# Kernel tuning notes

Hardware: AMD Instinct MI355X
Metric: run time of the kernel (lower is better)

The kernel has to match this reference:

```python
import jax, jax.numpy as jnp
import numpy as np

HEAD_SIZE = 64
INPUT_SIZE = 1024
B, T = 4, 4096


def setup_inputs() -> dict:
    key = jax.random.key(0)
    ks = jax.random.split(key, 7)
    s = 1.0 / np.sqrt(INPUT_SIZE)
    return {
        "x": jax.random.normal(ks[0], (B, T, INPUT_SIZE), dtype=jnp.float32),
        "Wk": jax.random.uniform(ks[1], (INPUT_SIZE, HEAD_SIZE), jnp.float32, -s, s),
        "bk": jax.random.uniform(ks[2], (HEAD_SIZE,), jnp.float32, -s, s),
        "Wq": jax.random.uniform(ks[3], (INPUT_SIZE, HEAD_SIZE), jnp.float32, -s, s),
        "bq": jax.random.uniform(ks[4], (HEAD_SIZE,), jnp.float32, -s, s),
        "Wv": jax.random.uniform(ks[5], (INPUT_SIZE, HEAD_SIZE), jnp.float32, -s, s),
        "bv": jax.random.uniform(ks[6], (HEAD_SIZE,), jnp.float32, -s, s),
    }


def reference(x, Wk, bk, Wq, bq, Wv, bv) -> jnp.ndarray:
    # x: [B, T, D]
    Tlen = x.shape[1]
    k = x @ Wk + bk          # [B, T, H]
    q = x @ Wq + bq          # [B, T, H]
    v = x @ Wv + bv          # [B, T, H]
    scale = 1.0 / jnp.sqrt(jnp.float32(HEAD_SIZE))
    # NOTE: original computes k @ q^T (not q @ k^T) -- keep that exact math.
    w = jnp.einsum("bth,bsh->bts", k, q) * scale  # [B, T, T]
    causal = jnp.tril(jnp.ones((Tlen, Tlen), dtype=bool))
    w = jnp.where(causal, w, -jnp.inf)
    w = jax.nn.softmax(w, axis=-1)
    out = jnp.einsum("bts,bsh->bth", w, v)        # [B, T, H]
    return out
```

## Files before the change

### kernel.cpp

```cpp
#include <hip/hip_runtime.h>
#include <hip/hip_bf16.h>
#include <stdint.h>

typedef __attribute__((ext_vector_type(8))) short short8;
typedef __attribute__((ext_vector_type(4))) float floatx4;

#define HD 64
#define D_IN 1024
#define TLEN 4096
#define NB 4
#define PPB 144
#define LDP 72
#define SL2E 0.18033688011112042f
#define WSZ 196608

__device__ __forceinline__ short f2bf(float f) {
    union { float f; uint32_t u; } v{f};
    uint32_t u = v.u;
    uint32_t r = (u + 0x7FFFu + ((u >> 16) & 1u)) >> 16;
    return (short)r;
}

__device__ __forceinline__ float bf2f(short s) {
    union { uint32_t u; float f; } v;
    v.u = ((uint32_t)(uint16_t)s) << 16;
    return v.f;
}

__device__ __forceinline__ uint32_t pk2(float a, float b) {
    __hip_bfloat162 h = __float22bfloat162_rn(float2{a, b});
    union { __hip_bfloat162 h; uint32_t u; } c{h};
    return c.u;
}

__device__ __forceinline__ void ld_lds16(const void* g, void* l) {
    __builtin_amdgcn_global_load_lds(
        (const __attribute__((address_space(1))) uint32_t*)g,
        (__attribute__((address_space(3))) uint32_t*)l, 16, 0, 0);
}

__global__ __launch_bounds__(256) void prep_w(const float* __restrict__ Wk,
                                              const float* __restrict__ Wq,
                                              const float* __restrict__ Wv,
                                              short* __restrict__ wt) {
    int i = blockIdx.x * 256 + threadIdx.x;
    int j  = i & 7;
    int l  = (i >> 3) & 63;
    int ks = (i >> 9) & 1;
    int rest = i >> 10;
    int f  = rest % 12;
    int kt = rest / 12;
    int mat = f >> 2, nt = f & 3;
    int n = nt * 16 + (l & 15);
    int k = kt * 64 + ks * 32 + (l >> 4) * 8 + j;
    const float* W = (mat == 0) ? Wk : ((mat == 1) ? Wq : Wv);
    wt[i] = f2bf(W[(size_t)k * 64 + n]);
}

__global__ __launch_bounds__(256) void proj(const float* __restrict__ x,
                                            const float* __restrict__ bk,
                                            const float* __restrict__ bq,
                                            const float* __restrict__ bv,
                                            const short* __restrict__ wt,
                                            short* __restrict__ ko,
                                            short* __restrict__ qo,
                                            short* __restrict__ vt) {
    __shared__ float xs[4][2048];

    int tid = threadIdx.x;
    int wave = tid >> 6, lane = tid & 63;
    int quad = lane >> 4, l16 = lane & 15;
    int row0 = blockIdx.x * 32;
    int wbase = tid & ~63;

    floatx4 acc[2][3];
#pragma unroll
    for (int mt = 0; mt < 2; mt++)
#pragma unroll
        for (int fi = 0; fi < 3; fi++) acc[mt][fi] = (floatx4){0.f, 0.f, 0.f, 0.f};

    auto stage = [&](int kt, int buf) {
#pragma unroll
        for (int it = 0; it < 2; it++) {
            int s = it * 256 + tid;
            int r = s >> 4, p = s & 15;
            int c = (((p >> 1) ^ (r & 7)) << 1) | (p & 1);
            ld_lds16(x + (size_t)(row0 + r) * D_IN + kt * 64 + c * 4,
                     &xs[buf][(it * 256 + wbase) * 4]);
        }
    };

    const short* wv0 = wt + (size_t)(((wave * 3) * 2) * 64 + lane) * 8;

    auto wload = [&](int kt, short8 (&wf)[3][2]) {
#pragma unroll
        for (int fi = 0; fi < 3; fi++)
#pragma unroll
            for (int ks = 0; ks < 2; ks++)
                wf[fi][ks] = *reinterpret_cast<const short8*>(
                    wv0 + (size_t)kt * 12288 + (size_t)((fi * 2 + ks) * 64) * 8);
    };

    auto body = [&](int kt, short8 (&wcur)[3][2]) {
        int buf = kt & 3;
#pragma unroll
        for (int ks = 0; ks < 2; ks++) {
            short8 av[2];
#pragma unroll
            for (int mt = 0; mt < 2; mt++) {
                int r = mt * 16 + l16;
                int g = ks * 4 + quad;
                const float4* pp = reinterpret_cast<const float4*>(
                    &xs[buf][r * 64 + ((g ^ (r & 7)) << 1) * 4]);
                float4 f0 = pp[0], f1 = pp[1];
                union { uint32_t u[4]; short8 s; } cv;
                cv.u[0] = pk2(f0.x, f0.y); cv.u[1] = pk2(f0.z, f0.w);
                cv.u[2] = pk2(f1.x, f1.y); cv.u[3] = pk2(f1.z, f1.w);
                av[mt] = cv.s;
            }
#pragma unroll
            for (int fi = 0; fi < 3; fi++)
#pragma unroll
                for (int mt = 0; mt < 2; mt++)
                    acc[mt][fi] = __builtin_amdgcn_mfma_f32_16x16x32_bf16(av[mt], wcur[fi][ks], acc[mt][fi], 0, 0, 0);
        }
    };

    short8 wA[3][2], wB[3][2];
    wload(0, wA);
    stage(0, 0); stage(1, 1); stage(2, 2);

    auto step = [&](int kt, short8 (&wcur)[3][2], short8 (&wnxt)[3][2]) {
        wload(kt + 1, wnxt);
        asm volatile("s_waitcnt vmcnt(8)" ::: "memory");
        __builtin_amdgcn_s_barrier();
        if (kt + 3 < 16) stage(kt + 3, (kt + 3) & 3);
        body(kt, wcur);
    };

    for (int kt2 = 0; kt2 < 14; kt2 += 2) {
        step(kt2, wA, wB);
        step(kt2 + 1, wB, wA);
    }
    wload(15, wB);
    asm volatile("s_waitcnt vmcnt(6)" ::: "memory");
    __builtin_amdgcn_s_barrier();
    body(14, wA);
    asm volatile("s_waitcnt vmcnt(0)" ::: "memory");
    __builtin_amdgcn_s_barrier();
    body(15, wB);

#pragma unroll
    for (int fi = 0; fi < 3; fi++) {
        int f = wave * 3 + fi;
        int mat = f >> 2, nt = f & 3;
        int col = nt * 16 + l16;
        const float* bias = (mat == 0) ? bk : ((mat == 1) ? bq : bv);
        float bb = bias[col];
#pragma unroll
        for (int mt = 0; mt < 2; mt++)
#pragma unroll
            for (int reg = 0; reg < 4; reg++) {
                float v = acc[mt][fi][reg] + bb;
                int row = row0 + mt * 16 + quad * 4 + reg;
                if (mat == 0) ko[(size_t)row * HD + col] = f2bf(v * SL2E);
                else if (mat == 1) qo[(size_t)row * HD + col] = f2bf(v);
                else {
                    int bt = row >> 12, tl = row & 4095;
                    vt[(size_t)bt * HD * TLEN + (size_t)col * TLEN + tl] = f2bf(v);
                }
            }
    }
}

template<int SPLIT>
__global__ __launch_bounds__(256) void attn_kern(const short* __restrict__ kb,
                                                 const short* __restrict__ qb,
                                                 const short* __restrict__ vtw,
                                                 short* __restrict__ pO,
                                                 float* __restrict__ pL,
                                                 float* __restrict__ out) {
    __shared__ short Ks[2][4096];
    __shared__ short Vs[2][4096];
    __shared__ short Ps[128 * LDP];

    int tid = threadIdx.x;
    int wave = tid >> 6, lane = tid & 63;
    int quad = lane >> 4, l16 = lane & 15;
    int wbase = tid & ~63;
    int batch = blockIdx.y;

    int tile, j0, j1, slot = 0, nparts = 1;
    if (SPLIT) {
        int bx = blockIdx.x;
        int t = 0, accb = 0;
        for (;;) { int p = (2 * t + 9) >> 3; if (bx < accb + p) break; accb += p; ++t; }
        tile = t;
        j0 = (bx - accb) * 8;
        int je = j0 + 8, lim = 2 * tile + 2;
        j1 = je < lim ? je : lim;
        slot = batch * PPB + bx;
        nparts = (2 * tile + 9) >> 3;
    } else {
        tile = 31 - blockIdx.x;
        j0 = 0; j1 = 2 * tile + 2;
    }
    int t0 = tile * 128;
    int jd = 2 * tile;
    size_t base = (size_t)batch * TLEN * HD;
    const short* vbase = vtw + (size_t)batch * HD * TLEN;

    short8 kf[2][2];
#pragma unroll
    for (int mt = 0; mt < 2; mt++) {
        int trow = t0 + wave * 32 + mt * 16 + l16;
#pragma unroll
        for (int ks = 0; ks < 2; ks++)
            kf[mt][ks] = *reinterpret_cast<const short8*>(kb + base + (size_t)trow * HD + ks * 32 + quad * 8);
    }

    floatx4 o_acc[2][4];
#pragma unroll
    for (int mt = 0; mt < 2; mt++)
#pragma unroll
        for (int ht = 0; ht < 4; ht++) o_acc[mt][ht] = (floatx4){0.f, 0.f, 0.f, 0.f};
    float l_p[2] = {0.f, 0.f};

    auto stage = [&](int j, int buf) {
        int s0 = j * 64;
#pragma unroll
        for (int it = 0; it < 2; it++) {
            int s = it * 256 + tid;
            int r = s >> 3, c = (s & 7) ^ (r & 7);
            ld_lds16(qb + base + (size_t)(s0 + r) * HD + c * 8,
                     &Ks[buf][(it * 256 + wbase) * 8]);
            ld_lds16(vbase + (size_t)r * TLEN + s0 + c * 8,
                     &Vs[buf][(it * 256 + wbase) * 8]);
        }
    };

    stage(j0, 0);
    for (int j = j0; j < j1; ++j) {
        int buf = (j - j0) & 1;
        __syncthreads();
        if (j + 1 < j1) stage(j + 1, buf ^ 1);

        if (j == jd + 1 && wave < 2) continue;

        floatx4 sacc[2][4];
#pragma unroll
        for (int mt = 0; mt < 2; mt++)
#pragma unroll
            for (int nt = 0; nt < 4; nt++) sacc[mt][nt] = (floatx4){0.f, 0.f, 0.f, 0.f};
#pragma unroll
        for (int ks = 0; ks < 2; ks++)
#pragma unroll
            for (int nt = 0; nt < 4; nt++) {
                int r = nt * 16 + l16, g = ks * 4 + quad;
                short8 a = *reinterpret_cast<const short8*>(
                    &Ks[buf][r * 64 + (g ^ (r & 7)) * 8]);
#pragma unroll
                for (int mt = 0; mt < 2; mt++)
                    sacc[mt][nt] = __builtin_amdgcn_mfma_f32_16x16x32_bf16(a, kf[mt][ks], sacc[mt][nt], 0, 0, 0);
            }

        float pv[2][4][4];
#pragma unroll
        for (int mt = 0; mt < 2; mt++)
#pragma unroll
            for (int nt = 0; nt < 4; nt++)
#pragma unroll
                for (int reg = 0; reg < 4; reg++)
                    pv[mt][nt][reg] = __builtin_amdgcn_exp2f(sacc[mt][nt][reg]);
        if (j >= jd) {
            int s0 = j * 64;
#pragma unroll
            for (int mt = 0; mt < 2; mt++) {
                int t_g = t0 + wave * 32 + mt * 16 + l16;
#pragma unroll
                for (int nt = 0; nt < 4; nt++) {
                    int s_g = s0 + nt * 16 + quad * 4;
#pragma unroll
                    for (int reg = 0; reg < 4; reg++)
                        if (s_g + reg > t_g) pv[mt][nt][reg] = 0.f;
                }
            }
        }
#pragma unroll
        for (int mt = 0; mt < 2; mt++) {
            l_p[mt] += ((pv[mt][0][0] + pv[mt][0][1]) + (pv[mt][0][2] + pv[mt][0][3]))
                     + ((pv[mt][1][0] + pv[mt][1][1]) + (pv[mt][1][2] + pv[mt][1][3]))
                     + ((pv[mt][2][0] + pv[mt][2][1]) + (pv[mt][2][2] + pv[mt][2][3]))
                     + ((pv[mt][3][0] + pv[mt][3][1]) + (pv[mt][3][2] + pv[mt][3][3]));
#pragma unroll
            for (int nt = 0; nt < 4; nt++) {
                union { uint32_t u[2]; uint64_t q; } w;
                w.u[0] = pk2(pv[mt][nt][0], pv[mt][nt][1]);
                w.u[1] = pk2(pv[mt][nt][2], pv[mt][nt][3]);
                int row = wave * 32 + mt * 16 + l16;
                *reinterpret_cast<uint64_t*>(&Ps[row * LDP + nt * 16 + quad * 4]) = w.q;
            }
        }

#pragma unroll
        for (int ks = 0; ks < 2; ks++) {
            short8 a[2];
#pragma unroll
            for (int mt = 0; mt < 2; mt++)
                a[mt] = *reinterpret_cast<const short8*>(
                    &Ps[(wave * 32 + mt * 16 + l16) * LDP + ks * 32 + quad * 8]);
#pragma unroll
            for (int ht = 0; ht < 4; ht++) {
                int r = ht * 16 + l16, g = ks * 4 + quad;
                short8 b = *reinterpret_cast<const short8*>(
                    &Vs[buf][r * 64 + (g ^ (r & 7)) * 8]);
#pragma unroll
                for (int mt = 0; mt < 2; mt++)
                    o_acc[mt][ht] = __builtin_amdgcn_mfma_f32_16x16x32_bf16(a[mt], b, o_acc[mt][ht], 0, 0, 0);
            }
        }
    }

#pragma unroll
    for (int mt = 0; mt < 2; mt++) {
        l_p[mt] += __shfl_xor(l_p[mt], 16);
        l_p[mt] += __shfl_xor(l_p[mt], 32);
    }

    if (SPLIT && nparts > 1) {
        short* po = pO + (size_t)slot * 8192;
#pragma unroll
        for (int mt = 0; mt < 2; mt++)
#pragma unroll
            for (int ht = 0; ht < 4; ht++)
#pragma unroll
                for (int reg = 0; reg < 4; reg++) {
                    int lr = wave * 32 + mt * 16 + quad * 4 + reg;
                    po[lr * 64 + ht * 16 + l16] = f2bf(o_acc[mt][ht][reg]);
                }
        if (quad == 0) {
#pragma unroll
            for (int mt = 0; mt < 2; mt++)
                pL[(size_t)slot * 128 + wave * 32 + mt * 16 + l16] = l_p[mt];
        }
    } else {
#pragma unroll
        for (int mt = 0; mt < 2; mt++) {
#pragma unroll
            for (int reg = 0; reg < 4; reg++) {
                float L = __shfl(l_p[mt], quad * 4 + reg, 64);
                float inv = 1.0f / L;
                int t = t0 + wave * 32 + mt * 16 + quad * 4 + reg;
#pragma unroll
                for (int ht = 0; ht < 4; ht++)
                    out[base + (size_t)t * HD + ht * 16 + l16] = o_acc[mt][ht][reg] * inv;
            }
        }
    }
}

__global__ __launch_bounds__(256) void attn_combine(const short* __restrict__ pO,
                                                    const float* __restrict__ pL,
                                                    float* __restrict__ out) {
    int tile = blockIdx.x + 4, batch = blockIdx.y, rq = blockIdx.z;
    int nparts = (2 * tile + 9) >> 3;
    int a = tile >> 2, r = tile & 3;
    int slot0 = batch * PPB + 2 * a * (a + 1) + r * (a + 1);
    int t = threadIdx.x;
    int off = rq * 2048 + t * 8;
    int row = off >> 6;
    int col0 = off & 63;

    float L = 0.f;
    float acc[8];
#pragma unroll
    for (int i = 0; i < 8; i++) acc[i] = 0.f;

    for (int p = 0; p < nparts; ++p) {
        int slot = slot0 + p;
        L += pL[(size_t)slot * 128 + row];
        short8 v = *reinterpret_cast<const short8*>(pO + (size_t)slot * 8192 + off);
#pragma unroll
        for (int i = 0; i < 8; i++) acc[i] += bf2f(v[i]);
    }
    float inv = 1.0f / L;
    float4* dstp = reinterpret_cast<float4*>(out + (size_t)batch * TLEN * HD +
                                             (size_t)(tile * 128 + row) * HD + col0);
#pragma unroll
    for (int c = 0; c < 2; c++) {
        float4 v;
        v.x = acc[c * 4 + 0] * inv; v.y = acc[c * 4 + 1] * inv;
        v.z = acc[c * 4 + 2] * inv; v.w = acc[c * 4 + 3] * inv;
        dstp[c] = v;
    }
}

extern "C" void kernel_launch(void* const* d_in, const int* in_sizes, int n_in,
                              void* d_out, int out_size, void* d_ws, size_t ws_size,
                              hipStream_t stream) {
    const float* x  = (const float*)d_in[0];
    const float* Wk = (const float*)d_in[1];
    const float* bk = (const float*)d_in[2];
    const float* Wq = (const float*)d_in[3];
    const float* bq = (const float*)d_in[4];
    const float* Wv = (const float*)d_in[5];
    const float* bv = (const float*)d_in[6];
    float* out = (float*)d_out;

    const size_t nrow = (size_t)NB * TLEN;
    short* ko = (short*)d_ws;
    short* qo = ko + nrow * HD;
    short* vt = qo + nrow * HD;
    short* wt = vt + nrow * HD;
    short* pO = wt + WSZ;
    float* pL = (float*)(pO + (size_t)NB * PPB * 8192);
    size_t need = (size_t)((char*)(pL + (size_t)NB * PPB * 128) - (char*)d_ws);

    prep_w<<<768, 256, 0, stream>>>(Wk, Wq, Wv, wt);
    proj<<<512, 256, 0, stream>>>(x, bk, bq, bv, wt, ko, qo, vt);
    if (ws_size >= need) {
        attn_kern<1><<<dim3(PPB, NB), 256, 0, stream>>>(ko, qo, vt, pO, pL, out);
        attn_combine<<<dim3(28, NB, 4), 256, 0, stream>>>(pO, pL, out);
    } else {
        attn_kern<0><<<dim3(32, NB), 256, 0, stream>>>(ko, qo, vt, nullptr, nullptr, out);
    }
}
```

Measured before the change: 149.8 us.

## Triple-buffer K/V tiles in attention with explicit vmcnt waits

Moves the attention kernel's K/V staging to dynamic shared memory with three slots and prefetches two tiles ahead instead of one. The __syncthreads is replaced by a targeted s_waitcnt vmcnt plus s_barrier so only the tile needed now must have landed. The aim is to hide more global load latency in the short per-block loops. In exchange it uses more LDS per block and depends on a hand-coded vmcnt count matching the number of loads issued per stage.

```diff
diff --git a/kernel.cpp b/kernel.cpp
--- a/kernel.cpp
+++ b/kernel.cpp
@@ -13,6 +13,7 @@
 #define LDP 72
 #define SL2E 0.18033688011112042f
 #define WSZ 196608
+#define ATTN_LDS (3 * 16384 + 128 * LDP * 2)
 
 __device__ __forceinline__ short f2bf(float f) {
     union { float f; uint32_t u; } v{f};
@@ -180,15 +181,14 @@
                                                  short* __restrict__ pO,
                                                  float* __restrict__ pL,
                                                  float* __restrict__ out) {
-    __shared__ short Ks[2][4096];
-    __shared__ short Vs[2][4096];
-    __shared__ short Ps[128 * LDP];
+    extern __shared__ char asmem[];
 
     int tid = threadIdx.x;
     int wave = tid >> 6, lane = tid & 63;
     int quad = lane >> 4, l16 = lane & 15;
     int wbase = tid & ~63;
     int batch = blockIdx.y;
+    short* Ps = (short*)(asmem + 3 * 16384);
 
     int tile, j0, j1, slot = 0, nparts = 1;
     if (SPLIT) {
@@ -226,99 +226,110 @@
         for (int ht = 0; ht < 4; ht++) o_acc[mt][ht] = (floatx4){0.f, 0.f, 0.f, 0.f};
     float l_p[2] = {0.f, 0.f};
 
-    auto stage = [&](int j, int buf) {
+    auto stage = [&](int j, int sl) {
+        short* Kd = (short*)(asmem + sl * 16384);
+        short* Vd = (short*)(asmem + sl * 16384 + 8192);
         int s0 = j * 64;
 #pragma unroll
         for (int it = 0; it < 2; it++) {
             int s = it * 256 + tid;
             int r = s >> 3, c = (s & 7) ^ (r & 7);
             ld_lds16(qb + base + (size_t)(s0 + r) * HD + c * 8,
-                     &Ks[buf][(it * 256 + wbase) * 8]);
+                     Kd + (it * 256 + wbase) * 8);
             ld_lds16(vbase + (size_t)r * TLEN + s0 + c * 8,
-                     &Vs[buf][(it * 256 + wbase) * 8]);
+                     Vd + (it * 256 + wbase) * 8);
         }
     };
 
     stage(j0, 0);
+    if (j0 + 1 < j1) stage(j0 + 1, 1);
+    int sl = 0, sn = 2;
     for (int j = j0; j < j1; ++j) {
-        int buf = (j - j0) & 1;
-        __syncthreads();
-        if (j + 1 < j1) stage(j + 1, buf ^ 1);
-
-        if (j == jd + 1 && wave < 2) continue;
-
-        floatx4 sacc[2][4];
-#pragma unroll
-        for (int mt = 0; mt < 2; mt++)
-#pragma unroll
-            for (int nt = 0; nt < 4; nt++) sacc[mt][nt] = (floatx4){0.f, 0.f, 0.f, 0.f};
-#pragma unroll
-        for (int ks = 0; ks < 2; ks++)
-#pragma unroll
-            for (int nt = 0; nt < 4; nt++) {
-                int r = nt * 16 + l16, g = ks * 4 + quad;
-                short8 a = *reinterpret_cast<const short8*>(
-                    &Ks[buf][r * 64 + (g ^ (r & 7)) * 8]);
+        if (j + 1 < j1) asm volatile("s_waitcnt vmcnt(4)" ::: "memory");
+        else            asm volatile("s_waitcnt vmcnt(0)" ::: "memory");
+        __builtin_amdgcn_s_barrier();
+        __builtin_amdgcn_sched_barrier(0);
+        if (j + 2 < j1) stage(j + 2, sn);
+
+        if (!(j == jd + 1 && wave < 2)) {
+            const short* Kc = (const short*)(asmem + sl * 16384);
+            const short* Vc = (const short*)(asmem + sl * 16384 + 8192);
+
+            floatx4 sacc[2][4];
+#pragma unroll
+            for (int mt = 0; mt < 2; mt++)
+#pragma unroll
+                for (int nt = 0; nt < 4; nt++) sacc[mt][nt] = (floatx4){0.f, 0.f, 0.f, 0.f};
+#pragma unroll
+            for (int ks = 0; ks < 2; ks++)
+#pragma unroll
+                for (int nt = 0; nt < 4; nt++) {
+                    int r = nt * 16 + l16, g = ks * 4 + quad;
+                    short8 a = *reinterpret_cast<const short8*>(
+                        Kc + r * 64 + (g ^ (r & 7)) * 8);
+#pragma unroll
+                    for (int mt = 0; mt < 2; mt++)
+                        sacc[mt][nt] = __builtin_amdgcn_mfma_f32_16x16x32_bf16(a, kf[mt][ks], sacc[mt][nt], 0, 0, 0);
+                }
+
+            float pv[2][4][4];
+#pragma unroll
+            for (int mt = 0; mt < 2; mt++)
+#pragma unroll
+                for (int nt = 0; nt < 4; nt++)
+#pragma unroll
+                    for (int reg = 0; reg < 4; reg++)
+                        pv[mt][nt][reg] = __builtin_amdgcn_exp2f(sacc[mt][nt][reg]);
+            if (j >= jd) {
+                int s0 = j * 64;
+#pragma unroll
+                for (int mt = 0; mt < 2; mt++) {
+                    int t_g = t0 + wave * 32 + mt * 16 + l16;
+#pragma unroll
+                    for (int nt = 0; nt < 4; nt++) {
+                        int s_g = s0 + nt * 16 + quad * 4;
+#pragma unroll
+                        for (int reg = 0; reg < 4; reg++)
+                            if (s_g + reg > t_g) pv[mt][nt][reg] = 0.f;
+                    }
+                }
+            }
+#pragma unroll
+            for (int mt = 0; mt < 2; mt++) {
+                l_p[mt] += ((pv[mt][0][0] + pv[mt][0][1]) + (pv[mt][0][2] + pv[mt][0][3]))
+                         + ((pv[mt][1][0] + pv[mt][1][1]) + (pv[mt][1][2] + pv[mt][1][3]))
+                         + ((pv[mt][2][0] + pv[mt][2][1]) + (pv[mt][2][2] + pv[mt][2][3]))
+                         + ((pv[mt][3][0] + pv[mt][3][1]) + (pv[mt][3][2] + pv[mt][3][3]));
+#pragma unroll
+                for (int nt = 0; nt < 4; nt++) {
+                    union { uint32_t u[2]; uint64_t q; } w;
+                    w.u[0] = pk2(pv[mt][nt][0], pv[mt][nt][1]);
+                    w.u[1] = pk2(pv[mt][nt][2], pv[mt][nt][3]);
+                    int row = wave * 32 + mt * 16 + l16;
+                    *reinterpret_cast<uint64_t*>(&Ps[row * LDP + nt * 16 + quad * 4]) = w.q;
+                }
+            }
+
+#pragma unroll
+            for (int ks = 0; ks < 2; ks++) {
+                short8 a[2];
 #pragma unroll
                 for (int mt = 0; mt < 2; mt++)
-                    sacc[mt][nt] = __builtin_amdgcn_mfma_f32_16x16x32_bf16(a, kf[mt][ks], sacc[mt][nt], 0, 0, 0);
-            }
-
-        float pv[2][4][4];
-#pragma unroll
-        for (int mt = 0; mt < 2; mt++)
-#pragma unroll
-            for (int nt = 0; nt < 4; nt++)
-#pragma unroll
-                for (int reg = 0; reg < 4; reg++)
-                    pv[mt][nt][reg] = __builtin_amdgcn_exp2f(sacc[mt][nt][reg]);
-        if (j >= jd) {
-            int s0 = j * 64;
-#pragma unroll
-            for (int mt = 0; mt < 2; mt++) {
-                int t_g = t0 + wave * 32 + mt * 16 + l16;
-#pragma unroll
-                for (int nt = 0; nt < 4; nt++) {
-                    int s_g = s0 + nt * 16 + quad * 4;
-#pragma unroll
-                    for (int reg = 0; reg < 4; reg++)
-                        if (s_g + reg > t_g) pv[mt][nt][reg] = 0.f;
-                }
-            }
-        }
-#pragma unroll
-        for (int mt = 0; mt < 2; mt++) {
-            l_p[mt] += ((pv[mt][0][0] + pv[mt][0][1]) + (pv[mt][0][2] + pv[mt][0][3]))
-                     + ((pv[mt][1][0] + pv[mt][1][1]) + (pv[mt][1][2] + pv[mt][1][3]))
-                     + ((pv[mt][2][0] + pv[mt][2][1]) + (pv[mt][2][2] + pv[mt][2][3]))
-                     + ((pv[mt][3][0] + pv[mt][3][1]) + (pv[mt][3][2] + pv[mt][3][3]));
-#pragma unroll
-            for (int nt = 0; nt < 4; nt++) {
-                union { uint32_t u[2]; uint64_t q; } w;
-                w.u[0] = pk2(pv[mt][nt][0], pv[mt][nt][1]);
-                w.u[1] = pk2(pv[mt][nt][2], pv[mt][nt][3]);
-                int row = wave * 32 + mt * 16 + l16;
-                *reinterpret_cast<uint64_t*>(&Ps[row * LDP + nt * 16 + quad * 4]) = w.q;
-            }
-        }
-
-#pragma unroll
-        for (int ks = 0; ks < 2; ks++) {
-            short8 a[2];
-#pragma unroll
-            for (int mt = 0; mt < 2; mt++)
-                a[mt] = *reinterpret_cast<const short8*>(
-                    &Ps[(wave * 32 + mt * 16 + l16) * LDP + ks * 32 + quad * 8]);
-#pragma unroll
-            for (int ht = 0; ht < 4; ht++) {
-                int r = ht * 16 + l16, g = ks * 4 + quad;
-                short8 b = *reinterpret_cast<const short8*>(
-                    &Vs[buf][r * 64 + (g ^ (r & 7)) * 8]);
-#pragma unroll
-                for (int mt = 0; mt < 2; mt++)
-                    o_acc[mt][ht] = __builtin_amdgcn_mfma_f32_16x16x32_bf16(a[mt], b, o_acc[mt][ht], 0, 0, 0);
-            }
-        }
+                    a[mt] = *reinterpret_cast<const short8*>(
+                        &Ps[(wave * 32 + mt * 16 + l16) * LDP + ks * 32 + quad * 8]);
+#pragma unroll
+                for (int ht = 0; ht < 4; ht++) {
+                    int r = ht * 16 + l16, g = ks * 4 + quad;
+                    short8 b = *reinterpret_cast<const short8*>(
+                        Vc + r * 64 + (g ^ (r & 7)) * 8);
+#pragma unroll
+                    for (int mt = 0; mt < 2; mt++)
+                        o_acc[mt][ht] = __builtin_amdgcn_mfma_f32_16x16x32_bf16(a[mt], b, o_acc[mt][ht], 0, 0, 0);
+                }
+            }
+        }
+        sl = (sl == 2) ? 0 : sl + 1;
+        sn = (sn == 2) ? 0 : sn + 1;
     }
 
 #pragma unroll
@@ -416,12 +427,23 @@
     float* pL = (float*)(pO + (size_t)NB * PPB * 8192);
     size_t need = (size_t)((char*)(pL + (size_t)NB * PPB * 128) - (char*)d_ws);
 
+    static int attr_set = 0;
+    if (!attr_set) {
+        (void)hipFuncSetAttribute((const void*)attn_kern<1>,
+                                  hipFuncAttributeMaxDynamicSharedMemorySize,
+                                  ATTN_LDS);
+        (void)hipFuncSetAttribute((const void*)attn_kern<0>,
+                                  hipFuncAttributeMaxDynamicSharedMemorySize,
+                                  ATTN_LDS);
+        attr_set = 1;
+    }
+
     prep_w<<<768, 256, 0, stream>>>(Wk, Wq, Wv, wt);
     proj<<<512, 256, 0, stream>>>(x, bk, bq, bv, wt, ko, qo, vt);
     if (ws_size >= need) {
-        attn_kern<1><<<dim3(PPB, NB), 256, 0, stream>>>(ko, qo, vt, pO, pL, out);
+        attn_kern<1><<<dim3(PPB, NB), 256, ATTN_LDS, stream>>>(ko, qo, vt, pO, pL, out);
         attn_combine<<<dim3(28, NB, 4), 256, 0, stream>>>(pO, pL, out);
     } else {
-        attn_kern<0><<<dim3(32, NB), 256, 0, stream>>>(ko, qo, vt, nullptr, nullptr, out);
-    }
-}
+        attn_kern<0><<<dim3(32, NB), 256, ATTN_LDS, stream>>>(ko, qo, vt, nullptr, nullptr, out);
+    }
+}
```

Result: slower. 153.0 us (+2.1%).
